# Kernel optimization log

Measured on AMD Instinct MI355X. Metric: run time of the kernel, lower is better.

## Reference

```python
import jax, jax.numpy as jnp
import numpy as np

EPS = 1e-07


def unfold(a, p):
    # torch F.unfold(a, p, padding=(p-1)//2, stride=1): [B,C,H,W] -> [B, C*p*p, H*W]
    B, C, H, W = a.shape
    pad = (p - 1) // 2
    ap = jnp.pad(a, ((0, 0), (0, 0), (pad, pad), (pad, pad)))
    # channel ordering is C-major then (kh, kw), matching torch unfold
    patches = jnp.stack([ap[:, :, i:i + H, j:j + W] for i in range(p) for j in range(p)], axis=2)
    return patches.reshape(B, C * p * p, H * W)


def linear_attn(q, k, x):
    # q:[B,h,l1,d1]  k:[B,h,l2,d1]  x:[B,h,l2,d2]
    l1, d1 = q.shape[-2:]
    l2, d2 = x.shape[-2:]
    kt = jnp.swapaxes(k, -2, -1)  # [B,h,d1,l2]
    if l1 * d1 * l2 + l1 * l2 * d2 <= d2 * l2 * d1 + d2 * d1 * l1:
        s = q @ kt                                        # [B,h,l1,l2]
        s = s / (s.sum(axis=-1, keepdims=True) + EPS)
        return s @ x
    else:
        out = q @ (kt @ x)                                # [B,h,l1,d2]
        denom = q @ kt.sum(axis=-1, keepdims=True) + EPS  # [B,h,l1,1]
        return out / denom


def setup_inputs() -> dict:
    key = jax.random.key(0)
    k1, k2, k3, k4, k5 = jax.random.split(key, 5)
    B, C, H, W = 4, 64, 128, 128
    x = jax.random.normal(k1, (B, C, H, W), dtype=jnp.float32)
    qkv_w = jax.random.normal(k2, (3 * C, C), dtype=jnp.float32) * 0.05
    qkv_b = jax.random.normal(k3, (3 * C,), dtype=jnp.float32) * 0.01
    proj_w = jax.random.normal(k4, (C, C, 3, 3), dtype=jnp.float32) * 0.05
    proj_b = jax.random.normal(k5, (C,), dtype=jnp.float32) * 0.01
    return {"x": x, "qkv_w": qkv_w, "qkv_b": qkv_b, "proj_w": proj_w, "proj_b": proj_b}


def reference(x, qkv_w, qkv_b, proj_w, proj_b):
    numHeads, patchSize = 8, 3
    B, C, H, W = x.shape
    L = H * W
    # 1x1 conv qkv
    qkv = jnp.einsum('bchw,oc->bohw', x, qkv_w) + qkv_b[None, :, None, None]
    q, k, v = qkv[:, :C], qkv[:, C:2 * C], qkv[:, 2 * C:]
    q = jax.nn.relu(q)
    k = jax.nn.relu(k)
    q = unfold(q, patchSize)  # [B, C*p*p, L]
    k = unfold(k, patchSize)
    v = v.reshape(B, C, L)
    d1 = C * patchSize * patchSize
    assert d1 % numHeads == 0  # chosen so replicate-pad branch is skipped
    q = jnp.swapaxes(q.reshape(B, numHeads, d1 // numHeads, L), -1, -2)   # [B,h,L,d1h]
    k = jnp.swapaxes(k.reshape(B, numHeads, d1 // numHeads, L), -1, -2)
    v = jnp.swapaxes(v.reshape(B, numHeads, C // numHeads, L), -1, -2)    # [B,h,L,d2h]
    out = linear_attn(q, k, v)                                            # [B,h,L,d2h]
    out = jnp.swapaxes(out, -1, -2).reshape(B, C, H, W)
    # 3x3 conv proj, padding 1
    out = jax.lax.conv_general_dilated(out, proj_w, window_strides=(1, 1), padding='SAME',
                                       dimension_numbers=('NCHW', 'OIHW', 'NCHW'))
    out = out + proj_b[None, :, None, None]
    return out
```

## Files before the change

### kernel.cpp

```cpp
#include <hip/hip_runtime.h>
#include <hip/hip_fp16.h>

#define LL 16384
#define HH 128
#define WW 128
#define CC 64
#define NH 8
#define EPSF 1e-7f
#define KVCHUNKS 32

typedef __attribute__((ext_vector_type(8))) _Float16 f16x8;
typedef __attribute__((ext_vector_type(4))) float f32x4;
typedef __attribute__((ext_vector_type(8))) unsigned short u16x8;

static __device__ __forceinline__ unsigned short f2h_bits(float v) {
    const _Float16 h = (_Float16)v;
    unsigned short b;
    __builtin_memcpy(&b, &h, 2);
    return b;
}
static __device__ __forceinline__ float h2f_u16(unsigned short s) {
    _Float16 h;
    __builtin_memcpy(&h, &s, 2);
    return (float)h;
}
static __device__ __forceinline__ float h2f_lo(unsigned int u) {
    return h2f_u16((unsigned short)(u & 0xffffu));
}
static __device__ __forceinline__ float h2f_hi(unsigned int u) {
    return h2f_u16((unsigned short)(u >> 16));
}

__global__ void qkv_kernel(const float* __restrict__ x, const float* __restrict__ w,
                           const float* __restrict__ bias,
                           unsigned short* __restrict__ q, unsigned short* __restrict__ k,
                           unsigned short* __restrict__ v) {
    const int pix0 = blockIdx.x * 128;
    const int b    = blockIdx.y;
    const int tid  = threadIdx.x;
    const int lane = tid & 63;
    const int wv   = tid >> 6;

    __shared__ _Float16 xh[128][72], xl[128][72];
    __shared__ unsigned short wspace[2 * 64 * 72];
    _Float16* whp = (_Float16*)wspace;
    _Float16* wlp = whp + 64 * 72;
    unsigned short* rep = wspace;

    {
        const float* xb = x + (size_t)b * CC * LL + pix0;
        for (int idx = tid; idx < 64 * 128; idx += 256) {
            const int ci = idx >> 7;
            const int px = idx & 127;
            const float vv = xb[(size_t)ci * LL + px];
            const _Float16 h = (_Float16)vv;
            xh[px][ci] = h;
            xl[px][ci] = (_Float16)(vv - (float)h);
        }
    }

    const int g8 = (lane >> 4) * 8;
    const int rl = lane & 15;

    for (int sec = 0; sec < 3; ++sec) {
        __syncthreads();
        {
            const float* wsec = w + (size_t)sec * 64 * 64;
            for (int idx = tid; idx < 64 * 64; idx += 256) {
                const int co = idx >> 6;
                const int ci = idx & 63;
                const float vv = wsec[co * 64 + ci];
                const _Float16 h = (_Float16)vv;
                whp[co * 72 + ci] = h;
                wlp[co * 72 + ci] = (_Float16)(vv - (float)h);
            }
        }
        __syncthreads();

        f32x4 acc[4][2];
#pragma unroll
        for (int ct = 0; ct < 4; ++ct)
#pragma unroll
            for (int pt = 0; pt < 2; ++pt) acc[ct][pt] = (f32x4)0.f;

#pragma unroll
        for (int ks = 0; ks < 2; ++ks) {
            const int kb = ks * 32 + g8;
            f16x8 ah[4], al[4], bh[2], bl[2];
#pragma unroll
            for (int ct = 0; ct < 4; ++ct) {
                ah[ct] = *(const f16x8*)&whp[(ct * 16 + rl) * 72 + kb];
                al[ct] = *(const f16x8*)&wlp[(ct * 16 + rl) * 72 + kb];
            }
#pragma unroll
            for (int pt = 0; pt < 2; ++pt) {
                bh[pt] = *(const f16x8*)&xh[wv * 32 + pt * 16 + rl][kb];
                bl[pt] = *(const f16x8*)&xl[wv * 32 + pt * 16 + rl][kb];
            }
#pragma unroll
            for (int ct = 0; ct < 4; ++ct)
#pragma unroll
                for (int pt = 0; pt < 2; ++pt) {
                    acc[ct][pt] = __builtin_amdgcn_mfma_f32_16x16x32_f16(ah[ct], bh[pt], acc[ct][pt], 0, 0, 0);
                    acc[ct][pt] = __builtin_amdgcn_mfma_f32_16x16x32_f16(ah[ct], bl[pt], acc[ct][pt], 0, 0, 0);
                    acc[ct][pt] = __builtin_amdgcn_mfma_f32_16x16x32_f16(al[ct], bh[pt], acc[ct][pt], 0, 0, 0);
                }
        }
        __syncthreads();

        const bool do_relu = (sec < 2);
#pragma unroll
        for (int ct = 0; ct < 4; ++ct) {
            const int co_b = ct * 16 + (lane >> 4) * 4;
#pragma unroll
            for (int pt = 0; pt < 2; ++pt) {
                const int pxl = wv * 32 + pt * 16 + rl;
#pragma unroll
                for (int j = 0; j < 4; ++j) {
                    const int co = co_b + j;
                    float val = acc[ct][pt][j] + bias[sec * 64 + co];
                    if (do_relu) val = fmaxf(val, 0.f);
                    rep[co * 128 + pxl] = f2h_bits(val);
                }
            }
        }
        __syncthreads();

        unsigned short* dst = ((sec == 0) ? q : (sec == 1) ? k : v) + (size_t)b * 64 * LL;
#pragma unroll
        for (int i = 0; i < 4; ++i) {
            const int slot = i * 256 + tid;
            const int co = slot >> 4;
            const int u4 = slot & 15;
            *(uint4*)(dst + (size_t)co * LL + pix0 + u4 * 8) = *(const uint4*)&rep[co * 128 + u4 * 8];
        }
    }
}

__global__ void kv_kernel(const unsigned short* __restrict__ k,
                          const unsigned short* __restrict__ v,
                          float* __restrict__ KVp) {
    const int chunk = blockIdx.x;
    const int h = blockIdx.y;
    const int b = blockIdx.z;
    const int tid = threadIdx.x;
    const int c  = tid >> 5;
    const int s  = tid & 31;
    const int half = s >> 4;
    const int sl   = s & 15;
    const int cpb  = half * 4;

    __shared__ float klds[8][6][130];

    {
        const unsigned short* kb = k + ((size_t)(b * 64) + 8 * h) * LL;
        for (int t = tid; t < 8 * 6 * 130; t += 256) {
            const int ch = t / 780;
            const int r1 = t - ch * 780;
            const int lr = r1 / 130;
            const int cx = r1 - lr * 130;
            const int gy = chunk * 4 + lr - 1;
            const int gx = cx - 1;
            const bool ok = (gy >= 0 && gy < HH && gx >= 0 && gx < WW);
            klds[ch][lr][cx] = ok ? h2f_u16(kb[(size_t)ch * LL + gy * WW + gx]) : 0.f;
        }
    }
    __syncthreads();

    const unsigned short* vbase = v + ((size_t)(b * 64) + 8 * h + cpb) * LL;

    float kv4[9][4] = {{0.f}};
    float ks[9] = {0.f};

    for (int r = 0; r < 4; ++r) {
        const int y = chunk * 4 + r;
        for (int g = 0; g < 4; ++g) {
            const int col0 = g * 32 + sl * 2;
            float va[4], vb2[4];
#pragma unroll
            for (int cp = 0; cp < 4; ++cp) {
                const unsigned int u = *(const unsigned int*)(vbase + (size_t)cp * LL + y * WW + col0);
                va[cp]  = h2f_lo(u);
                vb2[cp] = h2f_hi(u);
            }
            float kw[3][4];
#pragma unroll
            for (int dy = 0; dy < 3; ++dy)
#pragma unroll
                for (int dxx = 0; dxx < 4; ++dxx)
                    kw[dy][dxx] = klds[c][r + dy][col0 + dxx];
#pragma unroll
            for (int dy = 0; dy < 3; ++dy)
#pragma unroll
                for (int dx = 0; dx < 3; ++dx) {
                    const int p = dy * 3 + dx;
                    const float ka  = kw[dy][dx];
                    const float kb2 = kw[dy][dx + 1];
                    ks[p] += ka + kb2;
#pragma unroll
                    for (int cp = 0; cp < 4; ++cp)
                        kv4[p][cp] = fmaf(kb2, vb2[cp], fmaf(ka, va[cp], kv4[p][cp]));
                }
        }
    }

#pragma unroll
    for (int p = 0; p < 9; ++p) {
#pragma unroll
        for (int m = 8; m >= 1; m >>= 1) ks[p] += __shfl_xor(ks[p], m);
#pragma unroll
        for (int cp = 0; cp < 4; ++cp) {
#pragma unroll
            for (int m = 8; m >= 1; m >>= 1) kv4[p][cp] += __shfl_xor(kv4[p][cp], m);
        }
    }

    if (sl == 0) {
        float* dst = KVp + (((size_t)(b * NH + h) * KVCHUNKS) + chunk) * 648;
#pragma unroll
        for (int p = 0; p < 9; ++p) {
#pragma unroll
            for (int cp = 0; cp < 4; ++cp)
                dst[(c * 9 + p) * 8 + cpb + cp] = kv4[p][cp];
            if (half == 0) dst[576 + c * 9 + p] = ks[p];
        }
    }
}

__global__ void kv_finalize(const float* __restrict__ KVp,
                            float* __restrict__ KV, float* __restrict__ KS) {
    const int bh = blockIdx.x;
    const float* src = KVp + (size_t)bh * KVCHUNKS * 648;
    for (int idx = threadIdx.x; idx < 648; idx += 256) {
        float s0 = 0.f, s1 = 0.f, s2 = 0.f, s3 = 0.f;
#pragma unroll
        for (int ch = 0; ch < KVCHUNKS; ch += 4) {
            s0 += src[(ch + 0) * 648 + idx];
            s1 += src[(ch + 1) * 648 + idx];
            s2 += src[(ch + 2) * 648 + idx];
            s3 += src[(ch + 3) * 648 + idx];
        }
        const float sum = (s0 + s1) + (s2 + s3);
        if (idx < 576) KV[(size_t)bh * 576 + idx] = sum;
        else           KS[(size_t)bh * 72 + (idx - 576)] = sum;
    }
}

__global__ void attn_kernel(const unsigned short* __restrict__ q, const float* __restrict__ KV,
                            const float* __restrict__ KS, unsigned int* __restrict__ aofu) {
    const int y = blockIdx.x;
    const int h = blockIdx.y;
    const int b = blockIdx.z;
    const int t = threadIdx.x;

    float out0[8] = {0.f}, out1[8] = {0.f};
    float den0 = 0.f, den1 = 0.f;
    const int kvbase = (b * NH + h) * 8;
    const bool tlo = (t > 0), thi = (t < 63);

    for (int c = 0; c < 8; ++c) {
        const unsigned short* qc = q + ((size_t)(b * 64) + 8 * h + c) * LL;
        float qw[3][6];
#pragma unroll
        for (int dy = 0; dy < 3; ++dy) {
            const int yy = y + dy - 1;
            const bool yok = (yy >= 0 && yy < HH);
            const unsigned short* row = qc + yy * WW;
            const unsigned int u0 = (yok && tlo) ? *(const unsigned int*)(row + 2 * t - 2) : 0u;
            const unsigned int u1 = yok ? *(const unsigned int*)(row + 2 * t) : 0u;
            const unsigned int u2 = (yok && thi) ? *(const unsigned int*)(row + 2 * t + 2) : 0u;
            qw[dy][0] = h2f_lo(u0);  qw[dy][1] = h2f_hi(u0);
            qw[dy][2] = h2f_lo(u1);  qw[dy][3] = h2f_hi(u1);
            qw[dy][4] = h2f_lo(u2);  qw[dy][5] = h2f_hi(u2);
        }
        const float* kvr = KV + ((size_t)(kvbase + c) * 9) * 8;
        const float* ksr = KS + (size_t)(kvbase + c) * 9;
#pragma unroll
        for (int dy = 0; dy < 3; ++dy)
#pragma unroll
            for (int dx = 0; dx < 3; ++dx) {
                const int p = dy * 3 + dx;
                const float q0 = qw[dy][1 + dx];
                const float q1 = qw[dy][2 + dx];
                const float ksv = ksr[p];
                den0 = fmaf(q0, ksv, den0);
                den1 = fmaf(q1, ksv, den1);
#pragma unroll
                for (int cp = 0; cp < 8; ++cp) {
                    const float kvv = kvr[p * 8 + cp];
                    out0[cp] = fmaf(q0, kvv, out0[cp]);
                    out1[cp] = fmaf(q1, kvv, out1[cp]);
                }
            }
    }
    const float inv0 = 1.f / (den0 + EPSF);
    const float inv1 = 1.f / (den1 + EPSF);
    const int pixu = y * (WW / 2) + t;
#pragma unroll
    for (int cp = 0; cp < 8; ++cp) {
        const unsigned int lo = f2h_bits(out0[cp] * inv0);
        const unsigned int hi = f2h_bits(out1[cp] * inv1);
        aofu[((size_t)(b * 64) + h * 8 + cp) * (LL / 2) + pixu] = lo | (hi << 16);
    }
}

__global__ void wprep_kernel(const float* __restrict__ w, unsigned short* __restrict__ wfrag) {
    const int idx = blockIdx.x * 256 + threadIdx.x;
    const int k  = idx & 63;
    const int co = (idx >> 6) & 63;
    const int ks = idx >> 12;
    const int kg = ks * 64 + k;
    const int ci = kg >> 4, tap = kg & 15;
    const float vv = (tap < 9) ? w[(co * 64 + ci) * 9 + tap] : 0.f;
    const int kx = (((k >> 3) ^ (co & 7)) << 3) | (k & 7);
    wfrag[((size_t)ks * 64 + co) * 64 + kx] = f2h_bits(vv);
}

#define CONV_PREFETCH(KS)                                                        \
    do {                                                                         \
        const unsigned short* src_ = aofb + (size_t)((KS) * 4 + scis) * LL;      \
        pf0 = (oky0 && okxm) ? src_[offm - WW] : (unsigned short)0;              \
        pf1 = oky0 ? src_[off0 - WW] : (unsigned short)0;                        \
        pf2 = (oky0 && okxp) ? src_[offp - WW] : (unsigned short)0;              \
        pf3 = okxm ? src_[offm] : (unsigned short)0;                             \
        pf4 = src_[off0];                                                        \
        pf5 = okxp ? src_[offp] : (unsigned short)0;                             \
        pf6 = (oky2 && okxm) ? src_[offm + WW] : (unsigned short)0;              \
        pf7 = oky2 ? src_[off0 + WW] : (unsigned short)0;                        \
        pf8 = (oky2 && okxp) ? src_[offp + WW] : (unsigned short)0;              \
        const uint4* wsrc_ = (const uint4*)(wfrag + (size_t)(KS) * 4096);        \
        wf0 = wsrc_[tid];                                                        \
        wf1 = wsrc_[256 + tid];                                                  \
    } while (0)

__global__ __launch_bounds__(256) void conv_kernel(const unsigned short* __restrict__ aof,
                                                   const unsigned short* __restrict__ wfrag,
                                                   const float* __restrict__ bias,
                                                   float* __restrict__ out) {
    const int bid = blockIdx.x;
    const int swz = (bid & 7) * 128 + (bid >> 3);
    const int b = swz >> 8;
    const int rem = swz & 255;
    const int y = rem >> 1;
    const int colbase = (rem & 1) * 64;
    const int tid = threadIdx.x;
    const int lane = tid & 63;
    const int wv = tid >> 6;
    const int rl = lane & 15;
    const int g  = lane >> 4;

    __shared__ unsigned short plds[2][64 * 64];
    __shared__ unsigned short wlds[2][64 * 64];

    f32x4 acc[4];
#pragma unroll
    for (int ct = 0; ct < 4; ++ct) acc[ct] = (f32x4)0.f;

    const int spix = tid & 63;
    const int scis = tid >> 6;

    const unsigned short* aofb = aof + (size_t)b * 64 * LL;
    const int xc   = colbase + spix;
    const int off0 = y * WW + xc;
    const int offm = off0 - 1;
    const int offp = off0 + 1;
    const bool oky0 = (y > 0);
    const bool oky2 = (y < HH - 1);
    const bool okxm = (xc > 0);
    const bool okxp = (xc < WW - 1);
    const int xs0 = (((2 * scis)     ^ (spix & 7)) << 3);
    const int xs1 = (((2 * scis + 1) ^ (spix & 7)) << 3);

    unsigned short pf0, pf1, pf2, pf3, pf4, pf5, pf6, pf7, pf8;
    uint4 wf0, wf1;

    CONV_PREFETCH(0);

    for (int ks = 0; ks < 16; ++ks) {
        const int cur = ks & 1;
        {
            unsigned short h16[16];
            h16[0] = pf0;  h16[1] = pf1;  h16[2] = pf2;
            h16[3] = pf3;  h16[4] = pf4;  h16[5] = pf5;
            h16[6] = pf6;  h16[7] = pf7;  h16[8] = pf8;
#pragma unroll
            for (int j = 9; j < 16; ++j) h16[j] = 0;
            *(u16x8*)&plds[cur][spix * 64 + xs0] = *(u16x8*)&h16[0];
            *(u16x8*)&plds[cur][spix * 64 + xs1] = *(u16x8*)&h16[8];
            uint4* wdst = (uint4*)&wlds[cur][0];
            wdst[tid]       = wf0;
            wdst[256 + tid] = wf1;
        }
        __syncthreads();
        if (ks < 15) CONV_PREFETCH(ks + 1);

#pragma unroll
        for (int ksub = 0; ksub < 2; ++ksub) {
            const int xs = (((ksub * 4 + g) ^ (rl & 7)) << 3);
            const int row = wv * 16 + rl;
            const f16x8 bh = *(const f16x8*)&plds[cur][row * 64 + xs];
#pragma unroll
            for (int ct = 0; ct < 4; ++ct) {
                const int rowa = ct * 16 + rl;
                const f16x8 ah = *(const f16x8*)&wlds[cur][rowa * 64 + xs];
                acc[ct] = __builtin_amdgcn_mfma_f32_16x16x32_f16(ah, bh, acc[ct], 0, 0, 0);
            }
        }
    }

#pragma unroll
    for (int ct = 0; ct < 4; ++ct) {
        const int co_b = ct * 16 + g * 4;
        const int px = colbase + wv * 16 + rl;
#pragma unroll
        for (int j = 0; j < 4; ++j) {
            const int co = co_b + j;
            out[((size_t)b * 64 + co) * LL + y * WW + px] = acc[ct][j] + bias[co];
        }
    }
}

extern "C" void kernel_launch(void* const* d_in, const int* in_sizes, int n_in,
                              void* d_out, int out_size, void* d_ws, size_t ws_size,
                              hipStream_t stream) {
    const float* x      = (const float*)d_in[0];
    const float* qkv_w  = (const float*)d_in[1];
    const float* qkv_b  = (const float*)d_in[2];
    const float* proj_w = (const float*)d_in[3];
    const float* proj_b = (const float*)d_in[4];
    float* out = (float*)d_out;
    float* ws  = (float*)d_ws;

    const size_t n1 = (size_t)4 * 64 * LL;
    unsigned short* qb  = (unsigned short*)ws;
    unsigned short* kb  = (unsigned short*)(ws + n1);
    unsigned short* vb  = (unsigned short*)(ws + 2 * n1);
    unsigned short* aof = (unsigned short*)(ws + 3 * n1);
    float* KV   = ws + 4 * n1;
    float* KS   = KV + 4 * 8 * 8 * 9 * 8;
    float* KVp  = KS + 4 * 8 * 8 * 9;
    unsigned short* wfrag = (unsigned short*)(KVp + (size_t)32 * KVCHUNKS * 648);

    wprep_kernel<<<256, 256, 0, stream>>>(proj_w, wfrag);
    qkv_kernel<<<dim3(128, 4), 256, 0, stream>>>(x, qkv_w, qkv_b, qb, kb, vb);
    kv_kernel<<<dim3(KVCHUNKS, NH, 4), 256, 0, stream>>>(kb, vb, KVp);
    kv_finalize<<<32, 256, 0, stream>>>(KVp, KV, KS);
    attn_kernel<<<dim3(128, NH, 4), 64, 0, stream>>>(qb, KV, KS, (unsigned int*)aof);
    conv_kernel<<<1024, 256, 0, stream>>>(aof, wfrag, proj_b, out);
}
```

Before: 100.8 us.

## Merge weight prep into KV finalize and widen conv halo loads

After: 96.96 us. 1.04x faster.

```diff
diff --git a/kernel.cpp b/kernel.cpp
--- a/kernel.cpp
+++ b/kernel.cpp
@@ -227,22 +227,35 @@
     }
 }
 
-__global__ void kv_finalize(const float* __restrict__ KVp,
-                            float* __restrict__ KV, float* __restrict__ KS) {
-    const int bh = blockIdx.x;
-    const float* src = KVp + (size_t)bh * KVCHUNKS * 648;
-    for (int idx = threadIdx.x; idx < 648; idx += 256) {
-        float s0 = 0.f, s1 = 0.f, s2 = 0.f, s3 = 0.f;
-#pragma unroll
-        for (int ch = 0; ch < KVCHUNKS; ch += 4) {
-            s0 += src[(ch + 0) * 648 + idx];
-            s1 += src[(ch + 1) * 648 + idx];
-            s2 += src[(ch + 2) * 648 + idx];
-            s3 += src[(ch + 3) * 648 + idx];
-        }
-        const float sum = (s0 + s1) + (s2 + s3);
-        if (idx < 576) KV[(size_t)bh * 576 + idx] = sum;
-        else           KS[(size_t)bh * 72 + (idx - 576)] = sum;
+__global__ void prep_kernel(const float* __restrict__ KVp,
+                            float* __restrict__ KV, float* __restrict__ KS,
+                            const float* __restrict__ w, unsigned short* __restrict__ wfrag) {
+    if (blockIdx.x < 32) {
+        const int bh = blockIdx.x;
+        const float* src = KVp + (size_t)bh * KVCHUNKS * 648;
+        for (int idx = threadIdx.x; idx < 648; idx += 256) {
+            float s0 = 0.f, s1 = 0.f, s2 = 0.f, s3 = 0.f;
+#pragma unroll
+            for (int ch = 0; ch < KVCHUNKS; ch += 4) {
+                s0 += src[(ch + 0) * 648 + idx];
+                s1 += src[(ch + 1) * 648 + idx];
+                s2 += src[(ch + 2) * 648 + idx];
+                s3 += src[(ch + 3) * 648 + idx];
+            }
+            const float sum = (s0 + s1) + (s2 + s3);
+            if (idx < 576) KV[(size_t)bh * 576 + idx] = sum;
+            else           KS[(size_t)bh * 72 + (idx - 576)] = sum;
+        }
+    } else {
+        const int idx = (blockIdx.x - 32) * 256 + threadIdx.x;
+        const int kk = idx & 63;
+        const int co = (idx >> 6) & 63;
+        const int ks = idx >> 12;
+        const int kg = ks * 64 + kk;
+        const int ci = kg >> 4, tap = kg & 15;
+        const float vv = (tap < 9) ? w[(co * 64 + ci) * 9 + tap] : 0.f;
+        const int kx = (((kk >> 3) ^ (co & 7)) << 3) | (kk & 7);
+        wfrag[((size_t)ks * 64 + co) * 64 + kx] = f2h_bits(vv);
     }
 }
 
@@ -304,33 +317,24 @@
     }
 }
 
-__global__ void wprep_kernel(const float* __restrict__ w, unsigned short* __restrict__ wfrag) {
-    const int idx = blockIdx.x * 256 + threadIdx.x;
-    const int k  = idx & 63;
-    const int co = (idx >> 6) & 63;
-    const int ks = idx >> 12;
-    const int kg = ks * 64 + k;
-    const int ci = kg >> 4, tap = kg & 15;
-    const float vv = (tap < 9) ? w[(co * 64 + ci) * 9 + tap] : 0.f;
-    const int kx = (((k >> 3) ^ (co & 7)) << 3) | (k & 7);
-    wfrag[((size_t)ks * 64 + co) * 64 + kx] = f2h_bits(vv);
-}
-
 #define CONV_PREFETCH(KS)                                                        \
     do {                                                                         \
-        const unsigned short* src_ = aofb + (size_t)((KS) * 4 + scis) * LL;      \
-        pf0 = (oky0 && okxm) ? src_[offm - WW] : (unsigned short)0;              \
-        pf1 = oky0 ? src_[off0 - WW] : (unsigned short)0;                        \
-        pf2 = (oky0 && okxp) ? src_[offp - WW] : (unsigned short)0;              \
-        pf3 = okxm ? src_[offm] : (unsigned short)0;                             \
-        pf4 = src_[off0];                                                        \
-        pf5 = okxp ? src_[offp] : (unsigned short)0;                             \
-        pf6 = (oky2 && okxm) ? src_[offm + WW] : (unsigned short)0;              \
-        pf7 = oky2 ? src_[off0 + WW] : (unsigned short)0;                        \
-        pf8 = (oky2 && okxp) ? src_[offp + WW] : (unsigned short)0;              \
-        const uint4* wsrc_ = (const uint4*)(wfrag + (size_t)(KS) * 4096);        \
-        wf0 = wsrc_[tid];                                                        \
-        wf1 = wsrc_[256 + tid];                                                  \
+        if (tid < 128) {                                                         \
+            const unsigned short* src_ = aofb + (size_t)((KS) * 4 + scis) * LL;  \
+            pa0 = (oky0 && u0ok) ? *(const unsigned int*)(src_ + o_m - 2) : 0u;  \
+            pa1 = oky0 ? *(const unsigned int*)(src_ + o_m) : 0u;                \
+            pa2 = (oky0 && u2ok) ? *(const unsigned int*)(src_ + o_m + 2) : 0u;  \
+            pb0 = u0ok ? *(const unsigned int*)(src_ + o_c - 2) : 0u;            \
+            pb1 = *(const unsigned int*)(src_ + o_c);                            \
+            pb2 = u2ok ? *(const unsigned int*)(src_ + o_c + 2) : 0u;            \
+            pc0 = (oky2 && u0ok) ? *(const unsigned int*)(src_ + o_p - 2) : 0u;  \
+            pc1 = oky2 ? *(const unsigned int*)(src_ + o_p) : 0u;                \
+            pc2 = (oky2 && u2ok) ? *(const unsigned int*)(src_ + o_p + 2) : 0u;  \
+        } else {                                                                 \
+            const uint4* wsrc_ = (const uint4*)(wfrag + (size_t)(KS) * 4096);    \
+            wf0 = wsrc_[wt];        wf1 = wsrc_[128 + wt];                       \
+            wf2 = wsrc_[256 + wt];  wf3 = wsrc_[384 + wt];                       \
+        }                                                                        \
     } while (0)
 
 __global__ __launch_bounds__(256) void conv_kernel(const unsigned short* __restrict__ aof,
@@ -356,40 +360,53 @@
 #pragma unroll
     for (int ct = 0; ct < 4; ++ct) acc[ct] = (f32x4)0.f;
 
-    const int spix = tid & 63;
-    const int scis = tid >> 6;
+    const int pair = tid & 31;
+    const int scis = (tid >> 5) & 3;
+    const int wt   = tid & 127;
+    const int pxA  = pair * 2;
+    const int pxB  = pxA + 1;
 
     const unsigned short* aofb = aof + (size_t)b * 64 * LL;
-    const int xc   = colbase + spix;
-    const int off0 = y * WW + xc;
-    const int offm = off0 - 1;
-    const int offp = off0 + 1;
+    const int xc0 = colbase + pxA;
+    const int o_c = y * WW + xc0;
+    const int o_m = o_c - WW;
+    const int o_p = o_c + WW;
     const bool oky0 = (y > 0);
     const bool oky2 = (y < HH - 1);
-    const bool okxm = (xc > 0);
-    const bool okxp = (xc < WW - 1);
-    const int xs0 = (((2 * scis)     ^ (spix & 7)) << 3);
-    const int xs1 = (((2 * scis + 1) ^ (spix & 7)) << 3);
-
-    unsigned short pf0, pf1, pf2, pf3, pf4, pf5, pf6, pf7, pf8;
-    uint4 wf0, wf1;
+    const bool u0ok = (xc0 >= 2);
+    const bool u2ok = (xc0 + 3 < WW);
+    const int xsA0 = (((2 * scis)     ^ (pxA & 7)) << 3);
+    const int xsA1 = (((2 * scis + 1) ^ (pxA & 7)) << 3);
+    const int xsB0 = (((2 * scis)     ^ (pxB & 7)) << 3);
+    const int xsB1 = (((2 * scis + 1) ^ (pxB & 7)) << 3);
+
+    unsigned int pa0, pa1, pa2, pb0, pb1, pb2, pc0, pc1, pc2;
+    uint4 wf0, wf1, wf2, wf3;
 
     CONV_PREFETCH(0);
 
     for (int ks = 0; ks < 16; ++ks) {
         const int cur = ks & 1;
-        {
-            unsigned short h16[16];
-            h16[0] = pf0;  h16[1] = pf1;  h16[2] = pf2;
-            h16[3] = pf3;  h16[4] = pf4;  h16[5] = pf5;
-            h16[6] = pf6;  h16[7] = pf7;  h16[8] = pf8;
-#pragma unroll
-            for (int j = 9; j < 16; ++j) h16[j] = 0;
-            *(u16x8*)&plds[cur][spix * 64 + xs0] = *(u16x8*)&h16[0];
-            *(u16x8*)&plds[cur][spix * 64 + xs1] = *(u16x8*)&h16[8];
+        if (tid < 128) {
+            unsigned short ha[16], hb[16];
+            ha[0] = (unsigned short)(pa0 >> 16);      ha[1] = (unsigned short)(pa1 & 0xffffu);  ha[2] = (unsigned short)(pa1 >> 16);
+            ha[3] = (unsigned short)(pb0 >> 16);      ha[4] = (unsigned short)(pb1 & 0xffffu);  ha[5] = (unsigned short)(pb1 >> 16);
+            ha[6] = (unsigned short)(pc0 >> 16);      ha[7] = (unsigned short)(pc1 & 0xffffu);  ha[8] = (unsigned short)(pc1 >> 16);
+            hb[0] = (unsigned short)(pa1 & 0xffffu);  hb[1] = (unsigned short)(pa1 >> 16);      hb[2] = (unsigned short)(pa2 & 0xffffu);
+            hb[3] = (unsigned short)(pb1 & 0xffffu);  hb[4] = (unsigned short)(pb1 >> 16);      hb[5] = (unsigned short)(pb2 & 0xffffu);
+            hb[6] = (unsigned short)(pc1 & 0xffffu);  hb[7] = (unsigned short)(pc1 >> 16);      hb[8] = (unsigned short)(pc2 & 0xffffu);
+#pragma unroll
+            for (int j = 9; j < 16; ++j) { ha[j] = 0; hb[j] = 0; }
+            *(u16x8*)&plds[cur][pxA * 64 + xsA0] = *(u16x8*)&ha[0];
+            *(u16x8*)&plds[cur][pxA * 64 + xsA1] = *(u16x8*)&ha[8];
+            *(u16x8*)&plds[cur][pxB * 64 + xsB0] = *(u16x8*)&hb[0];
+            *(u16x8*)&plds[cur][pxB * 64 + xsB1] = *(u16x8*)&hb[8];
+        } else {
             uint4* wdst = (uint4*)&wlds[cur][0];
-            wdst[tid]       = wf0;
-            wdst[256 + tid] = wf1;
+            wdst[wt]        = wf0;
+            wdst[128 + wt]  = wf1;
+            wdst[256 + wt]  = wf2;
+            wdst[384 + wt]  = wf3;
         }
         __syncthreads();
         if (ks < 15) CONV_PREFETCH(ks + 1);
@@ -441,10 +458,9 @@
     float* KVp  = KS + 4 * 8 * 8 * 9;
     unsigned short* wfrag = (unsigned short*)(KVp + (size_t)32 * KVCHUNKS * 648);
 
-    wprep_kernel<<<256, 256, 0, stream>>>(proj_w, wfrag);
     qkv_kernel<<<dim3(128, 4), 256, 0, stream>>>(x, qkv_w, qkv_b, qb, kb, vb);
     kv_kernel<<<dim3(KVCHUNKS, NH, 4), 256, 0, stream>>>(kb, vb, KVp);
-    kv_finalize<<<32, 256, 0, stream>>>(KVp, KV, KS);
+    prep_kernel<<<288, 256, 0, stream>>>(KVp, KV, KS, proj_w, wfrag);
     attn_kernel<<<dim3(128, NH, 4), 64, 0, stream>>>(qb, KV, KS, (unsigned int*)aof);
     conv_kernel<<<1024, 256, 0, stream>>>(aof, wfrag, proj_b, out);
 }
```
